# Kernel tuning notes

Measured on AMD Instinct MI355X. Metric: run time of the kernel, lower is better.

## Reference

```python
import jax, jax.numpy as jnp
import numpy as np

B, IN_DIM, D, C = 16384, 1024, 256, 100


def setup_inputs() -> dict:
    key = jax.random.key(0)
    k1, k2, k3, k4 = jax.random.split(key, 4)
    x = jax.random.normal(k1, (B, IN_DIM), dtype=jnp.float32)
    W = jax.random.normal(k2, (IN_DIM, D), dtype=jnp.float32) * (1.0 / np.sqrt(IN_DIM))
    b = jax.random.normal(k3, (D,), dtype=jnp.float32) * 0.01
    P = jax.random.normal(k4, (C, D), dtype=jnp.float32)  # class prototypes [C, D]
    return {"x": x, "W": W, "b": b, "P": P}


def reference(x, W, b, P):
    # Encoder: Z = x @ W + b  -> [B, D]
    Z = x @ W + b
    d = Z.shape[-1]
    # MSE(r, p) = mean((r - p)^2) = (|r|^2 - 2 r.p + |p|^2) / D
    # Computed via expansion to avoid the [B, C, D] broadcast intermediate.
    sq = (
        jnp.sum(Z * Z, axis=-1, keepdims=True)      # [B, 1]
        - 2.0 * (Z @ P.T)                            # [B, C]
        + jnp.sum(P * P, axis=-1)[None, :]           # [1, C]
    )
    return -sq / d  # [B, C]
```

## Files before the change

### kernel.cpp

```cpp
#include <hip/hip_runtime.h>

#define BATCH 16384
#define KDIM  1024
#define DDIM  256
#define CNUM  100
#define CPAD  112

typedef __bf16 bf16x4 __attribute__((ext_vector_type(4)));
typedef __bf16 bf16x8 __attribute__((ext_vector_type(8)));
typedef float  floatx4 __attribute__((ext_vector_type(4)));

static __device__ __forceinline__ unsigned short f2b(float f) {
    return __builtin_bit_cast(unsigned short, (__bf16)f);
}

static __device__ __forceinline__ void gload_lds16(const unsigned short* g,
                                                   unsigned short* l) {
    __builtin_amdgcn_global_load_lds(
        (const __attribute__((address_space(1))) unsigned int*)g,
        (__attribute__((address_space(3))) unsigned int*)l, 16, 0, 0);
}

__global__ __launch_bounds__(256) void prep(const float* __restrict__ W,
                                            const float* __restrict__ P,
                                            unsigned short* __restrict__ Wt,
                                            unsigned short* __restrict__ Pbf,
                                            float* __restrict__ pnorm2) {
    __shared__ float T[32][33];
    const int bid = blockIdx.x;
    if (bid < 256) {
        const int k0 = (bid & 31) * 32;
        const int n0 = (bid >> 5) * 32;
        const int j  = threadIdx.x & 31;
        const int i0 = threadIdx.x >> 5;
#pragma unroll
        for (int l = 0; l < 4; ++l) {
            int i = i0 + l * 8;
            T[i][j] = W[(k0 + i) * DDIM + n0 + j];
        }
        __syncthreads();
#pragma unroll
        for (int l = 0; l < 4; ++l) {
            int i = i0 + l * 8;
            Wt[(n0 + i) * KDIM + k0 + j] = f2b(T[j][i]);
        }
    } else {
        const int wave = threadIdx.x >> 6;
        const int lane = threadIdx.x & 63;
        const int c = (bid - 256) * 4 + wave;
        float s = 0.f;
#pragma unroll
        for (int jj = 0; jj < 4; ++jj) {
            int d = jj * 64 + lane;
            float v = (c < CNUM) ? P[c * DDIM + d] : 0.f;
            Pbf[c * DDIM + d] = f2b(v);
            s += v * v;
        }
#pragma unroll
        for (int m = 1; m < 64; m <<= 1) s += __shfl_xor(s, m, 64);
        if (lane == 0) pnorm2[c] = s;
    }
}

__global__ __launch_bounds__(256, 2) void fused_main(
    const float* __restrict__ x, const float* __restrict__ bias,
    const unsigned short* __restrict__ Wt, const unsigned short* __restrict__ Pbf,
    const float* __restrict__ pnorm2, float* __restrict__ out)
{
    __shared__ unsigned short U[36864];
    unsigned short* Zs = U;
    __shared__ float rn2[4][32];

    const int tid  = threadIdx.x;
    const int wave = tid >> 6;
    const int lane = tid & 63;
    const int lm   = lane & 15;
    const int lq   = lane >> 4;
    const int r0   = blockIdx.x * 32;

    const int rowA = tid >> 3;
    const int kbA  = tid & 7;
    const float* gA = x + (r0 + rowA) * KDIM + kbA * 8;
    const int ldsA = rowA * 64 + ((kbA ^ (rowA & 7)) * 8);

    const int gkb = (lane & 7) ^ ((lane >> 3) & 7);
    const unsigned short* gB = Wt + (wave * 64 + (lane >> 3)) * KDIM + gkb * 8;

    const int sw0 = ((0 * 4 + lq) ^ (lm & 7)) * 8;
    const int sw1 = ((1 * 4 + lq) ^ (lm & 7)) * 8;

    floatx4 acc[2][4];
#pragma unroll
    for (int g = 0; g < 2; ++g)
#pragma unroll
        for (int f = 0; f < 4; ++f) { acc[g][f][0]=0.f; acc[g][f][1]=0.f; acc[g][f][2]=0.f; acc[g][f][3]=0.f; }

    {
        floatx4 q0 = *(const floatx4*)(gA);
        floatx4 q1 = *(const floatx4*)(gA + 4);
#pragma unroll
        for (int j = 0; j < 8; ++j)
            gload_lds16(gB + j * 8 * KDIM, U + 4096 + (wave * 64 + j * 8) * 64);
        bf16x8 ha;
        ha[0] = (__bf16)q0[0]; ha[1] = (__bf16)q0[1];
        ha[2] = (__bf16)q0[2]; ha[3] = (__bf16)q0[3];
        ha[4] = (__bf16)q1[0]; ha[5] = (__bf16)q1[1];
        ha[6] = (__bf16)q1[2]; ha[7] = (__bf16)q1[3];
        *(bf16x8*)&U[ldsA] = ha;
    }
    floatx4 pa0 = *(const floatx4*)(gA + 64);
    floatx4 pa1 = *(const floatx4*)(gA + 68);
    __syncthreads();

#pragma unroll 2
    for (int kk = 0; kk < KDIM; kk += 64) {
        const int cur = (kk >> 6) & 1;
        const int nxt = cur ^ 1;
        unsigned short* As_c = U + cur * 2048;
        unsigned short* Bs_c = U + 4096 + cur * 16384;
        if (kk + 64 < KDIM) {
            unsigned short* Bs_n = U + 4096 + nxt * 16384;
#pragma unroll
            for (int j = 0; j < 8; ++j)
                gload_lds16(gB + j * 8 * KDIM + kk + 64, Bs_n + (wave * 64 + j * 8) * 64);
            bf16x8 ha;
            ha[0] = (__bf16)pa0[0]; ha[1] = (__bf16)pa0[1];
            ha[2] = (__bf16)pa0[2]; ha[3] = (__bf16)pa0[3];
            ha[4] = (__bf16)pa1[0]; ha[5] = (__bf16)pa1[1];
            ha[6] = (__bf16)pa1[2]; ha[7] = (__bf16)pa1[3];
            *(bf16x8*)&(U + nxt * 2048)[ldsA] = ha;
            if (kk + 128 < KDIM) {
                pa0 = *(const floatx4*)(gA + kk + 128);
                pa1 = *(const floatx4*)(gA + kk + 132);
            }
        }
#pragma unroll
        for (int kf = 0; kf < 2; ++kf) {
            const int sw = kf ? sw1 : sw0;
            bf16x8 a0 = *(const bf16x8*)&As_c[lm * 64 + sw];
            bf16x8 a1 = *(const bf16x8*)&As_c[(16 + lm) * 64 + sw];
#pragma unroll
            for (int f = 0; f < 4; ++f) {
                bf16x8 bfr = *(const bf16x8*)&Bs_c[(wave * 64 + f * 16 + lm) * 64 + sw];
                acc[0][f] = __builtin_amdgcn_mfma_f32_16x16x32_bf16(a0, bfr, acc[0][f], 0, 0, 0);
                acc[1][f] = __builtin_amdgcn_mfma_f32_16x16x32_bf16(a1, bfr, acc[1][f], 0, 0, 0);
            }
        }
        __syncthreads();
    }

#pragma unroll
    for (int f = 0; f < 4; ++f) {
        float bb = bias[wave * 64 + f * 16 + lm];
#pragma unroll
        for (int g = 0; g < 2; ++g)
#pragma unroll
            for (int r = 0; r < 4; ++r) acc[g][f][r] += bb;
    }

#pragma unroll
    for (int g = 0; g < 2; ++g) {
        float s0 = 0.f, s1 = 0.f, s2 = 0.f, s3 = 0.f;
#pragma unroll
        for (int f = 0; f < 4; ++f) {
            s0 += acc[g][f][0] * acc[g][f][0];
            s1 += acc[g][f][1] * acc[g][f][1];
            s2 += acc[g][f][2] * acc[g][f][2];
            s3 += acc[g][f][3] * acc[g][f][3];
        }
#pragma unroll
        for (int m = 1; m < 16; m <<= 1) {
            s0 += __shfl_xor(s0, m, 64);
            s1 += __shfl_xor(s1, m, 64);
            s2 += __shfl_xor(s2, m, 64);
            s3 += __shfl_xor(s3, m, 64);
        }
        if (lm == 0) {
            int rl = g * 16 + lq * 4;
            rn2[wave][rl + 0] = s0;
            rn2[wave][rl + 1] = s1;
            rn2[wave][rl + 2] = s2;
            rn2[wave][rl + 3] = s3;
        }
    }

#pragma unroll
    for (int g = 0; g < 2; ++g)
#pragma unroll
        for (int f = 0; f < 4; ++f) {
            int col = wave * 64 + f * 16 + lm;
#pragma unroll
            for (int r = 0; r < 4; ++r)
                Zs[(g * 16 + lq * 4 + r) * 264 + col] = f2b(acc[g][f][r]);
        }
    __syncthreads();

#pragma unroll
    for (int t = 0; t < 2; ++t) {
        const int ct = wave * 2 + t;
        if (ct < 7) {
            floatx4 acc2[2];
#pragma unroll
            for (int nf = 0; nf < 2; ++nf) { acc2[nf][0]=0.f; acc2[nf][1]=0.f; acc2[nf][2]=0.f; acc2[nf][3]=0.f; }
            const unsigned short* gP = Pbf + (ct * 16 + lm) * DDIM + lq * 8;
#pragma unroll
            for (int ks = 0; ks < 8; ++ks) {
                bf16x8 ap = *(const bf16x8*)(gP + ks * 32);
#pragma unroll
                for (int nf = 0; nf < 2; ++nf) {
                    bf16x8 bz = *(const bf16x8*)&Zs[(nf * 16 + lm) * 264 + ks * 32 + lq * 8];
                    acc2[nf] = __builtin_amdgcn_mfma_f32_16x16x32_bf16(ap, bz, acc2[nf], 0, 0, 0);
                }
            }
            int c0 = ct * 16 + lq * 4;
            if (c0 < CNUM) {
                floatx4 pn = *(const floatx4*)(pnorm2 + c0);
#pragma unroll
                for (int nf = 0; nf < 2; ++nf) {
                    int rl = nf * 16 + lm;
                    float rn = rn2[0][rl] + rn2[1][rl] + rn2[2][rl] + rn2[3][rl];
                    floatx4 o;
#pragma unroll
                    for (int r = 0; r < 4; ++r)
                        o[r] = (2.f * acc2[nf][r] - rn - pn[r]) * (1.f / 256.f);
                    *(floatx4*)&out[(r0 + rl) * CNUM + c0] = o;
                }
            }
        }
    }
}

extern "C" void kernel_launch(void* const* d_in, const int* in_sizes, int n_in,
                              void* d_out, int out_size, void* d_ws, size_t ws_size,
                              hipStream_t stream) {
    const float* x = (const float*)d_in[0];
    const float* W = (const float*)d_in[1];
    const float* b = (const float*)d_in[2];
    const float* P = (const float*)d_in[3];
    float* out = (float*)d_out;

    unsigned short* Wt  = (unsigned short*)d_ws;
    unsigned short* Pbf = Wt + KDIM * DDIM;
    float* pn2 = (float*)(Pbf + CPAD * DDIM);

    prep<<<256 + CPAD / 4, 256, 0, stream>>>(W, P, Wt, Pbf, pn2);
    fused_main<<<BATCH / 32, 256, 0, stream>>>(x, b, Wt, Pbf, pn2, out);
}
```

Baseline: 117.1 us.

## Pre-pack W into MFMA fragment layout and load B operands directly to registers

```diff
diff --git a/kernel.cpp b/kernel.cpp
--- a/kernel.cpp
+++ b/kernel.cpp
@@ -6,7 +6,6 @@
 #define CNUM  100
 #define CPAD  112
 
-typedef __bf16 bf16x4 __attribute__((ext_vector_type(4)));
 typedef __bf16 bf16x8 __attribute__((ext_vector_type(8)));
 typedef float  floatx4 __attribute__((ext_vector_type(4)));
 
@@ -14,16 +13,9 @@
     return __builtin_bit_cast(unsigned short, (__bf16)f);
 }
 
-static __device__ __forceinline__ void gload_lds16(const unsigned short* g,
-                                                   unsigned short* l) {
-    __builtin_amdgcn_global_load_lds(
-        (const __attribute__((address_space(1))) unsigned int*)g,
-        (__attribute__((address_space(3))) unsigned int*)l, 16, 0, 0);
-}
-
 __global__ __launch_bounds__(256) void prep(const float* __restrict__ W,
                                             const float* __restrict__ P,
-                                            unsigned short* __restrict__ Wt,
+                                            unsigned short* __restrict__ Wt2,
                                             unsigned short* __restrict__ Pbf,
                                             float* __restrict__ pnorm2) {
     __shared__ float T[32][33];
@@ -39,10 +31,17 @@
             T[i][j] = W[(k0 + i) * DDIM + n0 + j];
         }
         __syncthreads();
-#pragma unroll
-        for (int l = 0; l < 4; ++l) {
-            int i = i0 + l * 8;
-            Wt[(n0 + i) * KDIM + k0 + j] = f2b(T[j][i]);
+        if (threadIdx.x < 128) {
+            const int l  = threadIdx.x & 63;
+            const int fn = threadIdx.x >> 6;
+            const int lm = l & 15, lq = l >> 4;
+            bf16x8 v;
+#pragma unroll
+            for (int jj = 0; jj < 8; ++jj)
+                v[jj] = (__bf16)T[lq * 8 + jj][fn * 16 + lm];
+            const int nblk = (n0 >> 4) + fn;
+            const int kblk = k0 >> 5;
+            *(bf16x8*)&Wt2[(nblk * 32 + kblk) * 512 + l * 8] = v;
         }
     } else {
         const int wave = threadIdx.x >> 6;
@@ -62,14 +61,53 @@
     }
 }
 
+#define KSTEP(KK, CUR, NXT)                                                    \
+    {                                                                          \
+        unsigned short* As_c = U + (CUR) * 2048;                               \
+        const int kb_ = (KK) >> 5;                                             \
+        if ((KK) + 64 < KDIM) {                                                \
+            _Pragma("unroll")                                                  \
+            for (int kf = 0; kf < 2; ++kf) {                                   \
+                _Pragma("unroll")                                              \
+                for (int f = 0; f < 4; ++f)                                    \
+                    b[NXT][kf][f] = *(const bf16x8*)(gB + f * 16384 +          \
+                                                     (kb_ + 2 + kf) * 512);    \
+            }                                                                  \
+            bf16x8 ha;                                                         \
+            ha[0] = (__bf16)pa0[0]; ha[1] = (__bf16)pa0[1];                    \
+            ha[2] = (__bf16)pa0[2]; ha[3] = (__bf16)pa0[3];                    \
+            ha[4] = (__bf16)pa1[0]; ha[5] = (__bf16)pa1[1];                    \
+            ha[6] = (__bf16)pa1[2]; ha[7] = (__bf16)pa1[3];                    \
+            *(bf16x8*)&(U + (NXT) * 2048)[ldsA] = ha;                          \
+            if ((KK) + 128 < KDIM) {                                           \
+                pa0 = *(const floatx4*)(gA + (KK) + 128);                      \
+                pa1 = *(const floatx4*)(gA + (KK) + 132);                      \
+            }                                                                  \
+        }                                                                      \
+        _Pragma("unroll")                                                      \
+        for (int kf = 0; kf < 2; ++kf) {                                       \
+            const int sw = kf ? sw1 : sw0;                                     \
+            bf16x8 a0 = *(const bf16x8*)&As_c[lm * 64 + sw];                   \
+            bf16x8 a1 = *(const bf16x8*)&As_c[(16 + lm) * 64 + sw];            \
+            _Pragma("unroll")                                                  \
+            for (int f = 0; f < 4; ++f) {                                      \
+                acc[0][f] = __builtin_amdgcn_mfma_f32_16x16x32_bf16(           \
+                    a0, b[CUR][kf][f], acc[0][f], 0, 0, 0);                    \
+                acc[1][f] = __builtin_amdgcn_mfma_f32_16x16x32_bf16(           \
+                    a1, b[CUR][kf][f], acc[1][f], 0, 0, 0);                    \
+            }                                                                  \
+        }                                                                      \
+        asm volatile("s_waitcnt lgkmcnt(0)\n\ts_barrier" ::: "memory");        \
+    }
+
 __global__ __launch_bounds__(256, 2) void fused_main(
     const float* __restrict__ x, const float* __restrict__ bias,
-    const unsigned short* __restrict__ Wt, const unsigned short* __restrict__ Pbf,
+    const unsigned short* __restrict__ Wt2, const unsigned short* __restrict__ Pbf,
     const float* __restrict__ pnorm2, float* __restrict__ out)
 {
-    __shared__ unsigned short U[36864];
+    __shared__ unsigned short U[8448];
+    __shared__ float rn2[4][32];
     unsigned short* Zs = U;
-    __shared__ float rn2[4][32];
 
     const int tid  = threadIdx.x;
     const int wave = tid >> 6;
@@ -83,8 +121,7 @@
     const float* gA = x + (r0 + rowA) * KDIM + kbA * 8;
     const int ldsA = rowA * 64 + ((kbA ^ (rowA & 7)) * 8);
 
-    const int gkb = (lane & 7) ^ ((lane >> 3) & 7);
-    const unsigned short* gB = Wt + (wave * 64 + (lane >> 3)) * KDIM + gkb * 8;
+    const unsigned short* gB = Wt2 + wave * 4 * 16384 + lane * 8;
 
     const int sw0 = ((0 * 4 + lq) ^ (lm & 7)) * 8;
     const int sw1 = ((1 * 4 + lq) ^ (lm & 7)) * 8;
@@ -94,13 +131,12 @@
     for (int g = 0; g < 2; ++g)
 #pragma unroll
         for (int f = 0; f < 4; ++f) { acc[g][f][0]=0.f; acc[g][f][1]=0.f; acc[g][f][2]=0.f; acc[g][f][3]=0.f; }
+
+    bf16x8 b[2][2][4];
 
     {
         floatx4 q0 = *(const floatx4*)(gA);
         floatx4 q1 = *(const floatx4*)(gA + 4);
-#pragma unroll
-        for (int j = 0; j < 8; ++j)
-            gload_lds16(gB + j * 8 * KDIM, U + 4096 + (wave * 64 + j * 8) * 64);
         bf16x8 ha;
         ha[0] = (__bf16)q0[0]; ha[1] = (__bf16)q0[1];
         ha[2] = (__bf16)q0[2]; ha[3] = (__bf16)q0[3];
@@ -108,45 +144,18 @@
         ha[6] = (__bf16)q1[2]; ha[7] = (__bf16)q1[3];
         *(bf16x8*)&U[ldsA] = ha;
     }
+#pragma unroll
+    for (int kf = 0; kf < 2; ++kf)
+#pragma unroll
+        for (int f = 0; f < 4; ++f)
+            b[0][kf][f] = *(const bf16x8*)(gB + f * 16384 + kf * 512);
     floatx4 pa0 = *(const floatx4*)(gA + 64);
     floatx4 pa1 = *(const floatx4*)(gA + 68);
-    __syncthreads();
-
-#pragma unroll 2
-    for (int kk = 0; kk < KDIM; kk += 64) {
-        const int cur = (kk >> 6) & 1;
-        const int nxt = cur ^ 1;
-        unsigned short* As_c = U + cur * 2048;
-        unsigned short* Bs_c = U + 4096 + cur * 16384;
-        if (kk + 64 < KDIM) {
-            unsigned short* Bs_n = U + 4096 + nxt * 16384;
-#pragma unroll
-            for (int j = 0; j < 8; ++j)
-                gload_lds16(gB + j * 8 * KDIM + kk + 64, Bs_n + (wave * 64 + j * 8) * 64);
-            bf16x8 ha;
-            ha[0] = (__bf16)pa0[0]; ha[1] = (__bf16)pa0[1];
-            ha[2] = (__bf16)pa0[2]; ha[3] = (__bf16)pa0[3];
-            ha[4] = (__bf16)pa1[0]; ha[5] = (__bf16)pa1[1];
-            ha[6] = (__bf16)pa1[2]; ha[7] = (__bf16)pa1[3];
-            *(bf16x8*)&(U + nxt * 2048)[ldsA] = ha;
-            if (kk + 128 < KDIM) {
-                pa0 = *(const floatx4*)(gA + kk + 128);
-                pa1 = *(const floatx4*)(gA + kk + 132);
-            }
-        }
-#pragma unroll
-        for (int kf = 0; kf < 2; ++kf) {
-            const int sw = kf ? sw1 : sw0;
-            bf16x8 a0 = *(const bf16x8*)&As_c[lm * 64 + sw];
-            bf16x8 a1 = *(const bf16x8*)&As_c[(16 + lm) * 64 + sw];
-#pragma unroll
-            for (int f = 0; f < 4; ++f) {
-                bf16x8 bfr = *(const bf16x8*)&Bs_c[(wave * 64 + f * 16 + lm) * 64 + sw];
-                acc[0][f] = __builtin_amdgcn_mfma_f32_16x16x32_bf16(a0, bfr, acc[0][f], 0, 0, 0);
-                acc[1][f] = __builtin_amdgcn_mfma_f32_16x16x32_bf16(a1, bfr, acc[1][f], 0, 0, 0);
-            }
-        }
-        __syncthreads();
+    asm volatile("s_waitcnt lgkmcnt(0)\n\ts_barrier" ::: "memory");
+
+    for (int kk0 = 0; kk0 < KDIM; kk0 += 128) {
+        KSTEP(kk0, 0, 1)
+        KSTEP(kk0 + 64, 1, 0)
     }
 
 #pragma unroll
@@ -239,10 +248,10 @@
     const float* P = (const float*)d_in[3];
     float* out = (float*)d_out;
 
-    unsigned short* Wt  = (unsigned short*)d_ws;
-    unsigned short* Pbf = Wt + KDIM * DDIM;
+    unsigned short* Wt2 = (unsigned short*)d_ws;
+    unsigned short* Pbf = Wt2 + KDIM * DDIM;
     float* pn2 = (float*)(Pbf + CPAD * DDIM);
 
-    prep<<<256 + CPAD / 4, 256, 0, stream>>>(W, P, Wt, Pbf, pn2);
-    fused_main<<<BATCH / 32, 256, 0, stream>>>(x, b, Wt, Pbf, pn2, out);
-}
+    prep<<<256 + CPAD / 4, 256, 0, stream>>>(W, P, Wt2, Pbf, pn2);
+    fused_main<<<BATCH / 32, 256, 0, stream>>>(x, b, Wt2, Pbf, pn2, out);
+}
```

Measured after the change: 116.1 us. Within noise of the previous version (-0.9%).
